# Kernel tuning notes

Hardware: AMD Instinct MI355X
Metric: run time of the kernel (lower is better)

## Reference

```python
import jax, jax.numpy as jnp
import numpy as np

N, MUL = 65536, 128          # nodes, multiplicity per irrep
SQRT3 = 1.7320508075688772   # CG component-normalization factors
SQRT2 = 1.4142135623730951


def setup_inputs() -> dict:
    key = jax.random.key(0)
    ks = jax.random.split(key, 8)
    return {
        "x0": jax.random.normal(ks[0], (N, MUL), jnp.float32),        # 128x0e
        "x1": jax.random.normal(ks[1], (N, MUL, 3), jnp.float32),     # 128x1o
        "y0": jax.random.normal(ks[2], (N, 1), jnp.float32),          # 1x0e
        "y1": jax.random.normal(ks[3], (N, 1, 3), jnp.float32),       # 1x1o
        "W0": jax.random.normal(ks[4], (2 * MUL, 3 * MUL), jnp.float32),  # 0e block: 256 -> 384 (256 gates + 128 scalars)
        "b0": jax.random.normal(ks[5], (3 * MUL,), jnp.float32) * 0.01,   # bias only on scalar (0e) outputs
        "W1o": jax.random.normal(ks[6], (2 * MUL, MUL), jnp.float32),     # 1o block: 256 -> 128
        "W1e": jax.random.normal(ks[7], (MUL, MUL), jnp.float32),         # 1e block: 128 -> 128
    }


def reference(x0, x1, y0, y1, W0, b0, W1o, W1e):
    # --- CG tensor product (e3nn 'component' normalization), x: 128x0e+128x1o, y: 1x0e+1x1o ---
    # 0e outputs: 0e*0e and 1o.1o (dot / sqrt(3))
    tp0 = jnp.concatenate(
        [x0 * y0, jnp.einsum("nci,ni->nc", x1, y1[:, 0, :]) / SQRT3], axis=-1
    )  # [N, 2*MUL]
    # 1o outputs: 0e x 1o and 1o x 0e
    tp1o = jnp.concatenate([x0[:, :, None] * y1, x1 * y0[:, :, None]], axis=1)  # [N, 2*MUL, 3]
    # 1e output: 1o x 1o cross product / sqrt(2)
    tp1e = jnp.cross(x1, y1) / SQRT2  # [N, MUL, 3]

    # --- irrep-wise block-diagonal Linear, 'element' path normalization (1/sqrt(fan_in)) ---
    s = tp0 @ W0 / jnp.sqrt(2.0 * MUL) + b0                          # [N, 3*MUL]
    v1o = jnp.einsum("nci,co->noi", tp1o, W1o) / jnp.sqrt(2.0 * MUL)  # [N, MUL, 3]
    v1e = jnp.einsum("nci,co->noi", tp1e, W1e) / jnp.sqrt(1.0 * MUL)  # [N, MUL, 3]

    # --- gate: prepended 256 even-scalar gates (sigmoid) gate the 1o/1e blocks; 128 scalars -> silu ---
    gates = jax.nn.sigmoid(s[:, : 2 * MUL])   # [N, 2*MUL]
    feats = jax.nn.silu(s[:, 2 * MUL :])      # [N, MUL]
    v1o = v1o * gates[:, :MUL, None]
    v1e = v1e * gates[:, MUL:, None]

    # concatenated IrrepsArray layout: 128x0e + 128x1o + 128x1e  -> [N, 128 + 384 + 384]
    n = feats.shape[0]
    return jnp.concatenate([feats, v1o.reshape(n, -1), v1e.reshape(n, -1)], axis=-1)
```

## Files before the change

kernel.cpp:

```cpp
#include <hip/hip_runtime.h>
#include <hip/hip_bf16.h>


typedef __bf16 bf16x8 __attribute__((ext_vector_type(8)));
typedef float f32x4 __attribute__((ext_vector_type(4)));
typedef unsigned short u16x8 __attribute__((ext_vector_type(8)));

#define W1OT_TOP 98304
#define W1OT_BOT 114688
#define W1ET     131072
#define INV16 0.0625f
#define INV_SQRT3 0.57735026918962576f

__device__ __forceinline__ unsigned short f2bf(float f) {
    unsigned u = __float_as_uint(f);
    u += 0x7FFFu + ((u >> 16) & 1u);
    return (unsigned short)(u >> 16);
}

__global__ __launch_bounds__(256) void prep_w(const float* __restrict__ W0,
                                              const float* __restrict__ W1o,
                                              const float* __restrict__ W1e,
                                              unsigned short* __restrict__ ws) {
    int idx = blockIdx.x * 256 + threadIdx.x;
    float v;
    if (idx < 98304) {
        int o = idx >> 8, k = idx & 255;
        v = W0[k * 384 + o];
    } else if (idx < 114688) {
        int j = idx - 98304; int o = j >> 7, k = j & 127;
        v = W1o[k * 128 + o];
    } else if (idx < 131072) {
        int j = idx - 114688; int o = j >> 7, k = j & 127;
        v = W1o[(128 + k) * 128 + o];
    } else {
        int j = idx - 131072; int o = j >> 7, k = j & 127;
        v = W1e[k * 128 + o];
    }
    ws[idx] = f2bf(v);
}

__global__ __launch_bounds__(256, 3) void tpl_gate(
    const float* __restrict__ x0, const float* __restrict__ x1,
    const float* __restrict__ y0, const float* __restrict__ y1,
    const float* __restrict__ b0, const unsigned short* __restrict__ ws,
    float* __restrict__ out) {
    __shared__ alignas(16) unsigned short sm[12288];
    __shared__ alignas(16) float ysm[64];
    __shared__ alignas(16) float b0sm[384];

    const int t = threadIdx.x;
    const int base = blockIdx.x * 16;

    {
        const int r = t >> 4, cg = t & 15, c0 = cg * 8;
        const int n = base + r;
        const int swz = (r & 7) * 8;
        const float w0v = y0[n];
        const float w1x = y1[n * 3 + 0], w1y = y1[n * 3 + 1], w1z = y1[n * 3 + 2];

        const float4* px = (const float4*)(x0 + (size_t)n * 128 + c0);
        float4 a4 = px[0], b4 = px[1];
        float xa[8] = {a4.x, a4.y, a4.z, a4.w, b4.x, b4.y, b4.z, b4.w};
        u16x8 q0, q1;
#pragma unroll
        for (int e = 0; e < 8; e++) { q0[e] = f2bf(xa[e]); q1[e] = f2bf(xa[e] * w0v); }
        *(u16x8*)(&sm[r * 128 + (c0 ^ swz)]) = q0;
        *(u16x8*)(&sm[8192 + r * 256 + (c0 ^ swz)]) = q1;

        const float4* p1 = (const float4*)(x1 + (size_t)n * 384 + c0 * 3);
        float xb[24];
#pragma unroll
        for (int e = 0; e < 6; e++) {
            float4 v = p1[e];
            xb[e * 4 + 0] = v.x; xb[e * 4 + 1] = v.y; xb[e * 4 + 2] = v.z; xb[e * 4 + 3] = v.w;
        }
        u16x8 qx, qy, qz, qt;
#pragma unroll
        for (int e = 0; e < 8; e++) {
            float vx = xb[e * 3 + 0], vy = xb[e * 3 + 1], vz = xb[e * 3 + 2];
            qx[e] = f2bf(vx); qy[e] = f2bf(vy); qz[e] = f2bf(vz);
            qt[e] = f2bf((vx * w1x + vy * w1y + vz * w1z) * INV_SQRT3);
        }
        *(u16x8*)(&sm[2048 + r * 128 + (c0 ^ swz)]) = qx;
        *(u16x8*)(&sm[4096 + r * 128 + (c0 ^ swz)]) = qy;
        *(u16x8*)(&sm[6144 + r * 128 + (c0 ^ swz)]) = qz;
        *(u16x8*)(&sm[8192 + r * 256 + ((128 + c0) ^ swz)]) = qt;

        if (t < 16) {
            int nn = base + t;
            ysm[t * 4 + 0] = y0[nn];
            ysm[t * 4 + 1] = y1[nn * 3 + 0];
            ysm[t * 4 + 2] = y1[nn * 3 + 1];
            ysm[t * 4 + 3] = y1[nn * 3 + 2];
        }
        if (t < 96) ((float4*)b0sm)[t] = ((const float4*)b0)[t];
    }
    __syncthreads();

    const int wave = t >> 6, lane = t & 63;
    const int cl = lane & 15, g4 = lane >> 4;
    const int swzr = (cl & 7) * 8;
    const int o0A = wave * 16;
    const int o0B = wave * 16 + 64;

    f32x4 accS[2][3], accP0[2], accP1[2][3], accQ[2][3];
#pragma unroll
    for (int p = 0; p < 2; p++) {
        accP0[p] = (f32x4)(0.0f);
#pragma unroll
        for (int g = 0; g < 3; g++) accS[p][g] = (f32x4)(0.0f);
#pragma unroll
        for (int i = 0; i < 3; i++) { accP1[p][i] = (f32x4)(0.0f); accQ[p][i] = (f32x4)(0.0f); }
    }
    const int oo[2] = {o0A, o0B};

#pragma unroll
    for (int ks = 0; ks < 8; ks++) {
        int eb = ks * 32 + g4 * 8;
        bf16x8 a = *(const bf16x8*)(&sm[8192 + cl * 256 + (eb ^ swzr)]);
#pragma unroll
        for (int p = 0; p < 2; p++) {
#pragma unroll
            for (int g = 0; g < 3; g++) {
                int row = g * 128 + oo[p] + cl;
                bf16x8 b = *(const bf16x8*)(&ws[row * 256 + eb]);
                accS[p][g] = __builtin_amdgcn_mfma_f32_16x16x32_bf16(b, a, accS[p][g], 0, 0, 0);
            }
        }
    }
#pragma unroll
    for (int k = 0; k < 4; k++) {
        int eb = k * 32 + g4 * 8;
        bf16x8 a0 = *(const bf16x8*)(&sm[0    + cl * 128 + (eb ^ swzr)]);
        bf16x8 ax = *(const bf16x8*)(&sm[2048 + cl * 128 + (eb ^ swzr)]);
        bf16x8 ay = *(const bf16x8*)(&sm[4096 + cl * 128 + (eb ^ swzr)]);
        bf16x8 az = *(const bf16x8*)(&sm[6144 + cl * 128 + (eb ^ swzr)]);
#pragma unroll
        for (int p = 0; p < 2; p++) {
            int row = oo[p] + cl;
            bf16x8 bt = *(const bf16x8*)(&ws[W1OT_TOP + row * 128 + eb]);
            bf16x8 bb = *(const bf16x8*)(&ws[W1OT_BOT + row * 128 + eb]);
            bf16x8 be = *(const bf16x8*)(&ws[W1ET     + row * 128 + eb]);
            accP0[p]    = __builtin_amdgcn_mfma_f32_16x16x32_bf16(bt, a0, accP0[p], 0, 0, 0);
            accP1[p][0] = __builtin_amdgcn_mfma_f32_16x16x32_bf16(bb, ax, accP1[p][0], 0, 0, 0);
            accP1[p][1] = __builtin_amdgcn_mfma_f32_16x16x32_bf16(bb, ay, accP1[p][1], 0, 0, 0);
            accP1[p][2] = __builtin_amdgcn_mfma_f32_16x16x32_bf16(bb, az, accP1[p][2], 0, 0, 0);
            accQ[p][0]  = __builtin_amdgcn_mfma_f32_16x16x32_bf16(be, ax, accQ[p][0], 0, 0, 0);
            accQ[p][1]  = __builtin_amdgcn_mfma_f32_16x16x32_bf16(be, ay, accQ[p][1], 0, 0, 0);
            accQ[p][2]  = __builtin_amdgcn_mfma_f32_16x16x32_bf16(be, az, accQ[p][2], 0, 0, 0);
        }
    }

    const float4 yv = ((const float4*)ysm)[cl];
    const float yy0 = yv.x, y1x = yv.y, y1y = yv.z, y1z = yv.w;
    float* orow = out + (size_t)(base + cl) * 896;
#pragma unroll
    for (int p = 0; p < 2; p++) {
        const int ob = oo[p] + g4 * 4;
        const float4 bq0 = *(const float4*)(&b0sm[ob]);
        const float4 bq1 = *(const float4*)(&b0sm[128 + ob]);
        const float4 bq2 = *(const float4*)(&b0sm[256 + ob]);
        const float* b0a = (const float*)&bq0;
        const float* b0b = (const float*)&bq1;
        const float* b0c = (const float*)&bq2;
        float feat4[4], vo[12], ve[12];
#pragma unroll
        for (int j = 0; j < 4; j++) {
            float s0 = accS[p][0][j] * INV16 + b0a[j];
            float s1 = accS[p][1][j] * INV16 + b0b[j];
            float s2 = accS[p][2][j] * INV16 + b0c[j];
            float g1o = INV16 / (1.0f + __expf(-s0));
            float g1e = INV16 / (1.0f + __expf(-s1));
            feat4[j] = s2 / (1.0f + __expf(-s2));
            float P0 = accP0[p][j];
            vo[j * 3 + 0] = (y1x * P0 + yy0 * accP1[p][0][j]) * g1o;
            vo[j * 3 + 1] = (y1y * P0 + yy0 * accP1[p][1][j]) * g1o;
            vo[j * 3 + 2] = (y1z * P0 + yy0 * accP1[p][2][j]) * g1o;
            ve[j * 3 + 0] = (y1z * accQ[p][1][j] - y1y * accQ[p][2][j]) * g1e;
            ve[j * 3 + 1] = (y1x * accQ[p][2][j] - y1z * accQ[p][0][j]) * g1e;
            ve[j * 3 + 2] = (y1y * accQ[p][0][j] - y1x * accQ[p][1][j]) * g1e;
        }
        *(float4*)(orow + ob) = *(const float4*)feat4;
#pragma unroll
        for (int tq = 0; tq < 3; tq++) {
            *(float4*)(orow + 128 + ob * 3 + tq * 4) = *(const float4*)(vo + tq * 4);
        }
#pragma unroll
        for (int tq = 0; tq < 3; tq++) {
            *(float4*)(orow + 512 + ob * 3 + tq * 4) = *(const float4*)(ve + tq * 4);
        }
    }
}

extern "C" void kernel_launch(void* const* d_in, const int* in_sizes, int n_in,
                              void* d_out, int out_size, void* d_ws, size_t ws_size,
                              hipStream_t stream) {
    (void)in_sizes; (void)n_in; (void)out_size; (void)ws_size;
    const float* x0  = (const float*)d_in[0];
    const float* x1  = (const float*)d_in[1];
    const float* y0  = (const float*)d_in[2];
    const float* y1  = (const float*)d_in[3];
    const float* W0  = (const float*)d_in[4];
    const float* b0  = (const float*)d_in[5];
    const float* W1o = (const float*)d_in[6];
    const float* W1e = (const float*)d_in[7];
    unsigned short* ws = (unsigned short*)d_ws;
    float* out = (float*)d_out;

    prep_w<<<dim3(576), dim3(256), 0, stream>>>(W0, W1o, W1e, ws);
    tpl_gate<<<dim3(65536 / 16), dim3(256), 0, stream>>>(x0, x1, y0, y1, b0, ws, out);
}
```

Measured before the change: 448.5 us.

## Retile to 32 nodes per 512-thread block and stage vector outputs through LDS

Each block now handles 32 nodes with 8 waves, and each wave owns a single 16-wide output slice for two 16-node groups. Each weight fragment is loaded once and reused across both node groups, which halves weight loads per node. The 1o and 1e results are staged through shared memory so each wave writes contiguous 48-float runs per node, improving global store coalescing. The cost is more shared memory (about 53 KB), extra barriers per node group, and lower occupancy bounds.

New measurement: 408.2 us. 9.0% less time.

```diff
diff --git a/kernel.cpp b/kernel.cpp
--- a/kernel.cpp
+++ b/kernel.cpp
@@ -40,20 +40,22 @@
     ws[idx] = f2bf(v);
 }
 
-__global__ __launch_bounds__(256, 3) void tpl_gate(
+__global__ __launch_bounds__(512, 2) void tpl_gate(
     const float* __restrict__ x0, const float* __restrict__ x1,
     const float* __restrict__ y0, const float* __restrict__ y1,
     const float* __restrict__ b0, const unsigned short* __restrict__ ws,
     float* __restrict__ out) {
-    __shared__ alignas(16) unsigned short sm[12288];
-    __shared__ alignas(16) float ysm[64];
+    __shared__ alignas(16) unsigned char smraw[53248];
+    __shared__ alignas(16) float ysm[128];
     __shared__ alignas(16) float b0sm[384];
+    unsigned short* sm = (unsigned short*)smraw;
+    float* smf = (float*)smraw;
 
     const int t = threadIdx.x;
-    const int base = blockIdx.x * 16;
+    const int base = blockIdx.x * 32;
 
     {
-        const int r = t >> 4, cg = t & 15, c0 = cg * 8;
+        const int r = t >> 4, c0 = (t & 15) * 8;
         const int n = base + r;
         const int swz = (r & 7) * 8;
         const float w0v = y0[n];
@@ -66,7 +68,7 @@
 #pragma unroll
         for (int e = 0; e < 8; e++) { q0[e] = f2bf(xa[e]); q1[e] = f2bf(xa[e] * w0v); }
         *(u16x8*)(&sm[r * 128 + (c0 ^ swz)]) = q0;
-        *(u16x8*)(&sm[8192 + r * 256 + (c0 ^ swz)]) = q1;
+        *(u16x8*)(&sm[16384 + r * 256 + (c0 ^ swz)]) = q1;
 
         const float4* p1 = (const float4*)(x1 + (size_t)n * 384 + c0 * 3);
         float xb[24];
@@ -82,12 +84,12 @@
             qx[e] = f2bf(vx); qy[e] = f2bf(vy); qz[e] = f2bf(vz);
             qt[e] = f2bf((vx * w1x + vy * w1y + vz * w1z) * INV_SQRT3);
         }
-        *(u16x8*)(&sm[2048 + r * 128 + (c0 ^ swz)]) = qx;
-        *(u16x8*)(&sm[4096 + r * 128 + (c0 ^ swz)]) = qy;
-        *(u16x8*)(&sm[6144 + r * 128 + (c0 ^ swz)]) = qz;
-        *(u16x8*)(&sm[8192 + r * 256 + ((128 + c0) ^ swz)]) = qt;
-
-        if (t < 16) {
+        *(u16x8*)(&sm[4096  + r * 128 + (c0 ^ swz)]) = qx;
+        *(u16x8*)(&sm[8192  + r * 128 + (c0 ^ swz)]) = qy;
+        *(u16x8*)(&sm[12288 + r * 128 + (c0 ^ swz)]) = qz;
+        *(u16x8*)(&sm[16384 + r * 256 + ((128 + c0) ^ swz)]) = qt;
+
+        if (t < 32) {
             int nn = base + t;
             ysm[t * 4 + 0] = y0[nn];
             ysm[t * 4 + 1] = y1[nn * 3 + 0];
@@ -98,98 +100,127 @@
     }
     __syncthreads();
 
-    const int wave = t >> 6, lane = t & 63;
+    const int w = t >> 6, lane = t & 63;
     const int cl = lane & 15, g4 = lane >> 4;
     const int swzr = (cl & 7) * 8;
-    const int o0A = wave * 16;
-    const int o0B = wave * 16 + 64;
+    const int ob = w * 16;
 
     f32x4 accS[2][3], accP0[2], accP1[2][3], accQ[2][3];
 #pragma unroll
-    for (int p = 0; p < 2; p++) {
-        accP0[p] = (f32x4)(0.0f);
-#pragma unroll
-        for (int g = 0; g < 3; g++) accS[p][g] = (f32x4)(0.0f);
-#pragma unroll
-        for (int i = 0; i < 3; i++) { accP1[p][i] = (f32x4)(0.0f); accQ[p][i] = (f32x4)(0.0f); }
-    }
-    const int oo[2] = {o0A, o0B};
+    for (int n = 0; n < 2; n++) {
+        accP0[n] = (f32x4)(0.0f);
+#pragma unroll
+        for (int g = 0; g < 3; g++) accS[n][g] = (f32x4)(0.0f);
+#pragma unroll
+        for (int i = 0; i < 3; i++) { accP1[n][i] = (f32x4)(0.0f); accQ[n][i] = (f32x4)(0.0f); }
+    }
 
 #pragma unroll
     for (int ks = 0; ks < 8; ks++) {
-        int eb = ks * 32 + g4 * 8;
-        bf16x8 a = *(const bf16x8*)(&sm[8192 + cl * 256 + (eb ^ swzr)]);
-#pragma unroll
-        for (int p = 0; p < 2; p++) {
-#pragma unroll
-            for (int g = 0; g < 3; g++) {
-                int row = g * 128 + oo[p] + cl;
-                bf16x8 b = *(const bf16x8*)(&ws[row * 256 + eb]);
-                accS[p][g] = __builtin_amdgcn_mfma_f32_16x16x32_bf16(b, a, accS[p][g], 0, 0, 0);
-            }
+        const int eb = ks * 32 + g4 * 8;
+        bf16x8 bw[3];
+#pragma unroll
+        for (int g = 0; g < 3; g++)
+            bw[g] = *(const bf16x8*)(&ws[(g * 128 + ob + cl) * 256 + eb]);
+#pragma unroll
+        for (int n = 0; n < 2; n++) {
+            bf16x8 a = *(const bf16x8*)(&sm[16384 + (16 * n + cl) * 256 + (eb ^ swzr)]);
+#pragma unroll
+            for (int g = 0; g < 3; g++)
+                accS[n][g] = __builtin_amdgcn_mfma_f32_16x16x32_bf16(bw[g], a, accS[n][g], 0, 0, 0);
         }
     }
 #pragma unroll
     for (int k = 0; k < 4; k++) {
-        int eb = k * 32 + g4 * 8;
-        bf16x8 a0 = *(const bf16x8*)(&sm[0    + cl * 128 + (eb ^ swzr)]);
-        bf16x8 ax = *(const bf16x8*)(&sm[2048 + cl * 128 + (eb ^ swzr)]);
-        bf16x8 ay = *(const bf16x8*)(&sm[4096 + cl * 128 + (eb ^ swzr)]);
-        bf16x8 az = *(const bf16x8*)(&sm[6144 + cl * 128 + (eb ^ swzr)]);
-#pragma unroll
-        for (int p = 0; p < 2; p++) {
-            int row = oo[p] + cl;
-            bf16x8 bt = *(const bf16x8*)(&ws[W1OT_TOP + row * 128 + eb]);
-            bf16x8 bb = *(const bf16x8*)(&ws[W1OT_BOT + row * 128 + eb]);
-            bf16x8 be = *(const bf16x8*)(&ws[W1ET     + row * 128 + eb]);
-            accP0[p]    = __builtin_amdgcn_mfma_f32_16x16x32_bf16(bt, a0, accP0[p], 0, 0, 0);
-            accP1[p][0] = __builtin_amdgcn_mfma_f32_16x16x32_bf16(bb, ax, accP1[p][0], 0, 0, 0);
-            accP1[p][1] = __builtin_amdgcn_mfma_f32_16x16x32_bf16(bb, ay, accP1[p][1], 0, 0, 0);
-            accP1[p][2] = __builtin_amdgcn_mfma_f32_16x16x32_bf16(bb, az, accP1[p][2], 0, 0, 0);
-            accQ[p][0]  = __builtin_amdgcn_mfma_f32_16x16x32_bf16(be, ax, accQ[p][0], 0, 0, 0);
-            accQ[p][1]  = __builtin_amdgcn_mfma_f32_16x16x32_bf16(be, ay, accQ[p][1], 0, 0, 0);
-            accQ[p][2]  = __builtin_amdgcn_mfma_f32_16x16x32_bf16(be, az, accQ[p][2], 0, 0, 0);
-        }
-    }
-
-    const float4 yv = ((const float4*)ysm)[cl];
-    const float yy0 = yv.x, y1x = yv.y, y1y = yv.z, y1z = yv.w;
-    float* orow = out + (size_t)(base + cl) * 896;
-#pragma unroll
-    for (int p = 0; p < 2; p++) {
-        const int ob = oo[p] + g4 * 4;
-        const float4 bq0 = *(const float4*)(&b0sm[ob]);
-        const float4 bq1 = *(const float4*)(&b0sm[128 + ob]);
-        const float4 bq2 = *(const float4*)(&b0sm[256 + ob]);
+        const int eb = k * 32 + g4 * 8;
+        bf16x8 bt = *(const bf16x8*)(&ws[W1OT_TOP + (ob + cl) * 128 + eb]);
+        bf16x8 bb = *(const bf16x8*)(&ws[W1OT_BOT + (ob + cl) * 128 + eb]);
+        bf16x8 be = *(const bf16x8*)(&ws[W1ET     + (ob + cl) * 128 + eb]);
+#pragma unroll
+        for (int n = 0; n < 2; n++) {
+            const int nr = 16 * n + cl;
+            bf16x8 a0 = *(const bf16x8*)(&sm[        nr * 128 + (eb ^ swzr)]);
+            bf16x8 ax = *(const bf16x8*)(&sm[4096  + nr * 128 + (eb ^ swzr)]);
+            bf16x8 ay = *(const bf16x8*)(&sm[8192  + nr * 128 + (eb ^ swzr)]);
+            bf16x8 az = *(const bf16x8*)(&sm[12288 + nr * 128 + (eb ^ swzr)]);
+            accP0[n]    = __builtin_amdgcn_mfma_f32_16x16x32_bf16(bt, a0, accP0[n], 0, 0, 0);
+            accP1[n][0] = __builtin_amdgcn_mfma_f32_16x16x32_bf16(bb, ax, accP1[n][0], 0, 0, 0);
+            accP1[n][1] = __builtin_amdgcn_mfma_f32_16x16x32_bf16(bb, ay, accP1[n][1], 0, 0, 0);
+            accP1[n][2] = __builtin_amdgcn_mfma_f32_16x16x32_bf16(bb, az, accP1[n][2], 0, 0, 0);
+            accQ[n][0]  = __builtin_amdgcn_mfma_f32_16x16x32_bf16(be, ax, accQ[n][0], 0, 0, 0);
+            accQ[n][1]  = __builtin_amdgcn_mfma_f32_16x16x32_bf16(be, ay, accQ[n][1], 0, 0, 0);
+            accQ[n][2]  = __builtin_amdgcn_mfma_f32_16x16x32_bf16(be, az, accQ[n][2], 0, 0, 0);
+        }
+    }
+
+    __syncthreads();
+
+    float* Ro = smf + w * 832;
+    float* Re = smf + 6656 + w * 832;
+
+#pragma unroll
+    for (int n = 0; n < 2; n++) {
+        const int node = 16 * n + cl;
+        const float4 yv = ((const float4*)ysm)[node];
+        const float yy0 = yv.x, y1x = yv.y, y1y = yv.z, y1z = yv.w;
+        const int o4 = ob + g4 * 4;
+        const float4 bq0 = *(const float4*)(&b0sm[o4]);
+        const float4 bq1 = *(const float4*)(&b0sm[128 + o4]);
+        const float4 bq2 = *(const float4*)(&b0sm[256 + o4]);
         const float* b0a = (const float*)&bq0;
         const float* b0b = (const float*)&bq1;
         const float* b0c = (const float*)&bq2;
-        float feat4[4], vo[12], ve[12];
+        float4 featq, vo4[3], ve4[3];
+        float* feat4 = (float*)&featq;
+        float* vo = (float*)vo4;
+        float* ve = (float*)ve4;
 #pragma unroll
         for (int j = 0; j < 4; j++) {
-            float s0 = accS[p][0][j] * INV16 + b0a[j];
-            float s1 = accS[p][1][j] * INV16 + b0b[j];
-            float s2 = accS[p][2][j] * INV16 + b0c[j];
+            float s0 = accS[n][0][j] * INV16 + b0a[j];
+            float s1 = accS[n][1][j] * INV16 + b0b[j];
+            float s2 = accS[n][2][j] * INV16 + b0c[j];
             float g1o = INV16 / (1.0f + __expf(-s0));
             float g1e = INV16 / (1.0f + __expf(-s1));
             feat4[j] = s2 / (1.0f + __expf(-s2));
-            float P0 = accP0[p][j];
-            vo[j * 3 + 0] = (y1x * P0 + yy0 * accP1[p][0][j]) * g1o;
-            vo[j * 3 + 1] = (y1y * P0 + yy0 * accP1[p][1][j]) * g1o;
-            vo[j * 3 + 2] = (y1z * P0 + yy0 * accP1[p][2][j]) * g1o;
-            ve[j * 3 + 0] = (y1z * accQ[p][1][j] - y1y * accQ[p][2][j]) * g1e;
-            ve[j * 3 + 1] = (y1x * accQ[p][2][j] - y1z * accQ[p][0][j]) * g1e;
-            ve[j * 3 + 2] = (y1y * accQ[p][0][j] - y1x * accQ[p][1][j]) * g1e;
-        }
-        *(float4*)(orow + ob) = *(const float4*)feat4;
-#pragma unroll
-        for (int tq = 0; tq < 3; tq++) {
-            *(float4*)(orow + 128 + ob * 3 + tq * 4) = *(const float4*)(vo + tq * 4);
-        }
-#pragma unroll
-        for (int tq = 0; tq < 3; tq++) {
-            *(float4*)(orow + 512 + ob * 3 + tq * 4) = *(const float4*)(ve + tq * 4);
-        }
+            float P0 = accP0[n][j];
+            vo[j * 3 + 0] = (y1x * P0 + yy0 * accP1[n][0][j]) * g1o;
+            vo[j * 3 + 1] = (y1y * P0 + yy0 * accP1[n][1][j]) * g1o;
+            vo[j * 3 + 2] = (y1z * P0 + yy0 * accP1[n][2][j]) * g1o;
+            ve[j * 3 + 0] = (y1z * accQ[n][1][j] - y1y * accQ[n][2][j]) * g1e;
+            ve[j * 3 + 1] = (y1x * accQ[n][2][j] - y1z * accQ[n][0][j]) * g1e;
+            ve[j * 3 + 2] = (y1y * accQ[n][0][j] - y1x * accQ[n][1][j]) * g1e;
+        }
+        *(float4*)(out + (size_t)(base + node) * 896 + o4) = featq;
+
+        {
+            float* wo = Ro + cl * 52 + g4 * 12;
+            float* we = Re + cl * 52 + g4 * 12;
+            ((float4*)wo)[0] = vo4[0];
+            ((float4*)wo)[1] = vo4[1];
+            ((float4*)wo)[2] = vo4[2];
+            ((float4*)we)[0] = ve4[0];
+            ((float4*)we)[1] = ve4[1];
+            ((float4*)we)[2] = ve4[2];
+        }
+        __syncthreads();
+
+#pragma unroll
+        for (int m = 0; m < 3; m++) {
+            int piece = m * 64 + lane;
+            int nd = (int)((unsigned)piece / 12u);
+            int kk = piece - nd * 12;
+            float4 v = *(const float4*)(Ro + nd * 52 + kk * 4);
+            *(float4*)(out + (size_t)(base + 16 * n + nd) * 896 + 128 + w * 48 + kk * 4) = v;
+        }
+#pragma unroll
+        for (int m = 0; m < 3; m++) {
+            int piece = m * 64 + lane;
+            int nd = (int)((unsigned)piece / 12u);
+            int kk = piece - nd * 12;
+            float4 v = *(const float4*)(Re + nd * 52 + kk * 4);
+            *(float4*)(out + (size_t)(base + 16 * n + nd) * 896 + 512 + w * 48 + kk * 4) = v;
+        }
+        __syncthreads();
     }
 }
 
@@ -209,5 +240,5 @@
     float* out = (float*)d_out;
 
     prep_w<<<dim3(576), dim3(256), 0, stream>>>(W0, W1o, W1e, ws);
-    tpl_gate<<<dim3(65536 / 16), dim3(256), 0, stream>>>(x0, x1, y0, y1, b0, ws, out);
-}
+    tpl_gate<<<dim3(65536 / 32), dim3(512), 0, stream>>>(x0, x1, y0, y1, b0, ws, out);
+}
```
